# Kernel tuning notes

Hardware: AMD Instinct MI355X
Metric: run time of the kernel (lower is better)

## Reference

```python
import jax, jax.numpy as jnp
import numpy as np

N_NODES = 8192
N_EDGES = 32768
D = 768
H1 = 8
NEG_SLOPE = 0.2


def setup_inputs() -> dict:
    key = jax.random.key(0)
    ks = jax.random.split(key, 10)
    s = 0.02  # init scale keeps attention logits numerically tame
    x = jax.random.normal(ks[0], (N_NODES, D), dtype=jnp.float32)
    edge_index = jax.random.randint(ks[1], (2, N_EDGES), 0, N_NODES, dtype=jnp.int64)
    W1 = jax.random.normal(ks[2], (D, H1 * D), dtype=jnp.float32) * s
    a_src1 = jax.random.normal(ks[3], (H1, D), dtype=jnp.float32) * s
    a_dst1 = jax.random.normal(ks[4], (H1, D), dtype=jnp.float32) * s
    b1 = jnp.zeros((H1 * D,), dtype=jnp.float32)
    W2 = jax.random.normal(ks[5], (H1 * D, D), dtype=jnp.float32) * s
    a_src2 = jax.random.normal(ks[6], (1, D), dtype=jnp.float32) * s
    a_dst2 = jax.random.normal(ks[7], (1, D), dtype=jnp.float32) * s
    b2 = jnp.zeros((D,), dtype=jnp.float32)
    return {"x": x, "edge_index": edge_index, "W1": W1, "a_src1": a_src1,
            "a_dst1": a_dst1, "b1": b1, "W2": W2, "a_src2": a_src2,
            "a_dst2": a_dst2, "b2": b2}


def gat_conv(x, src, dst, W, a_src, a_dst, b, heads, out_ch):
    """PyG GATConv (concat=True, self-loops already appended to src/dst)."""
    n = x.shape[0]
    h = (x @ W).reshape(n, heads, out_ch)            # [N,H,C]
    alpha_src = jnp.einsum("nhc,hc->nh", h, a_src)  # [N,H]
    alpha_dst = jnp.einsum("nhc,hc->nh", h, a_dst)  # [N,H]
    # edge scores: leaky_relu(a_src.h_j + a_dst.h_i) for edge j->i
    e = jax.nn.leaky_relu(alpha_src[src] + alpha_dst[dst], NEG_SLOPE)  # [E,H]
    # segment softmax over incoming edges of each destination node
    m = jax.ops.segment_max(e, dst, num_segments=n)   # [N,H]
    m = jnp.where(jnp.isfinite(m), m, 0.0)
    p = jnp.exp(e - m[dst])                           # [E,H]
    denom = jax.ops.segment_sum(p, dst, num_segments=n)
    alpha = p / denom[dst]                            # [E,H]
    msg = h[src] * alpha[:, :, None]                  # [E,H,C] gather+weight
    out = jax.ops.segment_sum(msg, dst, num_segments=n)  # [N,H,C] scatter-add
    return out.reshape(n, heads * out_ch) + b


def reference(x, edge_index, W1, a_src1, a_dst1, b1, W2, a_src2, a_dst2, b2):
    n = x.shape[0]
    loops = jnp.arange(n, dtype=edge_index.dtype)
    src = jnp.concatenate([edge_index[0], loops])  # add_self_loops=True
    dst = jnp.concatenate([edge_index[1], loops])
    h = gat_conv(x, src, dst, W1, a_src1, a_dst1, b1, H1, D)
    h = jax.nn.elu(h)
    out = gat_conv(h, src, dst, W2, a_src2, a_dst2, b2, 1, D)
    return out
```

## Files before the change

### kernel.cpp

```cpp
#include <hip/hip_runtime.h>
#include <hip/hip_bf16.h>


#define N_NODES 8192
#define N_EDGES 32768
#define E_TOT   (N_EDGES + N_NODES)
#define D_IN    768
#define H1      8
#define HC1     (H1 * D_IN)
#define KSPLIT  4
#define KSLICE  (HC1 / KSPLIT)

typedef unsigned short ushort_t;
using short8  = __attribute__((ext_vector_type(8))) short;
using short4v = __attribute__((ext_vector_type(4))) short;
using floatx4 = __attribute__((ext_vector_type(4))) float;

__device__ __forceinline__ float bf2f(unsigned short u) {
  return __uint_as_float(((unsigned)u) << 16);
}
__device__ __forceinline__ unsigned short f2bf(float f) {
  unsigned u = __float_as_uint(f);
  unsigned r = (u + 0x7fffu + ((u >> 16) & 1u)) >> 16;
  return (unsigned short)r;
}

__device__ __forceinline__ void gll16(const ushort_t* g, ushort_t* l) {
  __builtin_amdgcn_global_load_lds(
      (const __attribute__((address_space(1))) void*)g,
      (__attribute__((address_space(3))) void*)l, 16, 0, 0);
}

__global__ __launch_bounds__(256) void frag_transpose_kernel(
    const float* __restrict__ W, ushort_t* __restrict__ out,
    int Kdim, int Ndim) {
  __shared__ float lds[64 * 65];
  const int bx = blockIdx.x;
  const int by = blockIdx.y;
  const int tid = threadIdx.x;
  const int n0 = bx * 64, k0 = by * 64;
  const int nn = tid & 63, kq = tid >> 6;
#pragma unroll
  for (int it = 0; it < 16; ++it) {
    int kk = it * 4 + kq;
    lds[kk * 65 + nn] = W[(size_t)(k0 + kk) * Ndim + n0 + nn];
  }
  __syncthreads();
  const int Ksub = Kdim >> 5;
#pragma unroll
  for (int it = 0; it < 2; ++it) {
    int idx = tid + 256 * it;
    int c = idx >> 6, l = idx & 63;
    int cn = c >> 1, ck = c & 1;
    int lrow = l & 15, lq = l >> 4;
    int n_loc = cn * 16 + lrow;
    int kb = ck * 32 + lq * 8;
    ushort_t v[8];
#pragma unroll
    for (int e = 0; e < 8; ++e) v[e] = f2bf(lds[(kb + e) * 65 + n_loc]);
    size_t chunk = (size_t)(bx * 4 + cn) * Ksub + (by * 2 + ck);
    *(short8*)(out + chunk * 512 + l * 8) = *(short8*)v;
  }
}

__global__ void prep_aw_kernel(const float* __restrict__ W1,
                               const float* __restrict__ aS,
                               const float* __restrict__ aD,
                               float* __restrict__ awS,
                               float* __restrict__ awD) {
  const int d = blockIdx.x;
  const int t = threadIdx.x;
  const float* row = W1 + (size_t)d * HC1;
  float ps[H1], pd[H1];
#pragma unroll
  for (int h = 0; h < H1; ++h) { ps[h] = 0.f; pd[h] = 0.f; }
#pragma unroll
  for (int h = 0; h < H1; ++h)
#pragma unroll
    for (int j = 0; j < 3; ++j) {
      int idx = h * 768 + j * 256 + t;
      float w = row[idx];
      ps[h] += w * aS[idx];
      pd[h] += w * aD[idx];
    }
#pragma unroll
  for (int h = 0; h < H1; ++h)
    for (int off = 32; off > 0; off >>= 1) {
      ps[h] += __shfl_down(ps[h], off, 64);
      pd[h] += __shfl_down(pd[h], off, 64);
    }
  __shared__ float red[2][4][H1];
  int w = t >> 6;
  if ((t & 63) == 0) {
#pragma unroll
    for (int h = 0; h < H1; ++h) { red[0][w][h] = ps[h]; red[1][w][h] = pd[h]; }
  }
  __syncthreads();
  if (t < H1)
    awS[d * H1 + t] = red[0][0][t] + red[0][1][t] + red[0][2][t] + red[0][3][t];
  else if (t >= 64 && t < 64 + H1) {
    int h = t - 64;
    awD[d * H1 + h] = red[1][0][h] + red[1][1][h] + red[1][2][h] + red[1][3][h];
  }
}

__global__ void node_prep_kernel(const float* __restrict__ x,
                                 const float* __restrict__ awS,
                                 const float* __restrict__ awD,
                                 ushort_t* __restrict__ xb,
                                 float* __restrict__ as1,
                                 float* __restrict__ ad1) {
  const int n = blockIdx.x;
  const int t = threadIdx.x;
  float ps[H1], pd[H1];
#pragma unroll
  for (int h = 0; h < H1; ++h) { ps[h] = 0.f; pd[h] = 0.f; }
#pragma unroll
  for (int j = 0; j < 3; ++j) {
    int d = j * 256 + t;
    float xv = x[(size_t)n * 768 + d];
    xb[(size_t)n * 768 + d] = f2bf(xv);
    const float4* s4 = (const float4*)(awS + d * 8);
    const float4* d4 = (const float4*)(awD + d * 8);
    float4 a0 = s4[0], a1 = s4[1];
    float4 c0 = d4[0], c1 = d4[1];
    ps[0] += xv * a0.x; ps[1] += xv * a0.y; ps[2] += xv * a0.z; ps[3] += xv * a0.w;
    ps[4] += xv * a1.x; ps[5] += xv * a1.y; ps[6] += xv * a1.z; ps[7] += xv * a1.w;
    pd[0] += xv * c0.x; pd[1] += xv * c0.y; pd[2] += xv * c0.z; pd[3] += xv * c0.w;
    pd[4] += xv * c1.x; pd[5] += xv * c1.y; pd[6] += xv * c1.z; pd[7] += xv * c1.w;
  }
#pragma unroll
  for (int h = 0; h < H1; ++h)
    for (int off = 32; off > 0; off >>= 1) {
      ps[h] += __shfl_down(ps[h], off, 64);
      pd[h] += __shfl_down(pd[h], off, 64);
    }
  __shared__ float red[2][4][H1];
  int w = t >> 6;
  if ((t & 63) == 0) {
#pragma unroll
    for (int h = 0; h < H1; ++h) { red[0][w][h] = ps[h]; red[1][w][h] = pd[h]; }
  }
  __syncthreads();
  if (t < H1)
    as1[n * H1 + t] = red[0][0][t] + red[0][1][t] + red[0][2][t] + red[0][3][t];
  else if (t >= 64 && t < 64 + H1) {
    int h = t - 64;
    ad1[n * H1 + h] = red[1][0][h] + red[1][1][h] + red[1][2][h] + red[1][3][h];
  }
}

__global__ void deg_kernel(const int* __restrict__ dst, int* __restrict__ deg) {
  int e = blockIdx.x * blockDim.x + threadIdx.x;
  if (e >= E_TOT) return;
  int d = (e < N_EDGES) ? dst[e] : (e - N_EDGES);
  atomicAdd(&deg[d], 1);
}

__global__ void scan_kernel(const int* __restrict__ deg, int* __restrict__ start,
                            int* __restrict__ cursor) {
  __shared__ int sums[1024];
  int t = threadIdx.x;
  int base = t * 8;
  int local[8];
  int s = 0;
#pragma unroll
  for (int i = 0; i < 8; ++i) { local[i] = s; s += deg[base + i]; }
  sums[t] = s;
  __syncthreads();
  for (int off = 1; off < 1024; off <<= 1) {
    int v = (t >= off) ? sums[t - off] : 0;
    __syncthreads();
    sums[t] += v;
    __syncthreads();
  }
  int excl = (t == 0) ? 0 : sums[t - 1];
#pragma unroll
  for (int i = 0; i < 8; ++i) {
    int st = excl + local[i];
    start[base + i] = st;
    cursor[base + i] = st;
  }
}

__global__ void fill_kernel(const int* __restrict__ dst, int* __restrict__ cursor,
                            int* __restrict__ csr) {
  int e = blockIdx.x * blockDim.x + threadIdx.x;
  if (e >= E_TOT) return;
  int d = (e < N_EDGES) ? dst[e] : (e - N_EDGES);
  int pos = atomicAdd(&cursor[d], 1);
  csr[pos] = e;
}

__global__ __launch_bounds__(256) void attn1_kernel(
    const ushort_t* __restrict__ xb, const float* __restrict__ as1,
    const float* __restrict__ ad1, const int* __restrict__ start,
    const int* __restrict__ deg, const int* __restrict__ csr,
    const int* __restrict__ src, ushort_t* __restrict__ z_sw) {
  const int n = blockIdx.x;
  const int t = threadIdx.x;
  const int st = start[n], dg = deg[n];
  const int h = t & 7, eloc = t >> 3;
  __shared__ float invd[H1];
  __shared__ float alphaS[16][H1];
  __shared__ int sidx[16];
  __shared__ float red[4][H1];
  __shared__ uint4 xs[16 * 96];

  const float adv = ad1[n * H1 + h];
  float pden = 0.f;
  for (int base = 0; base < dg; base += 32) {
    int ei = base + eloc;
    if (ei < dg) {
      int e = csr[st + ei];
      int s = (e < N_EDGES) ? src[e] : (e - N_EDGES);
      float l = as1[s * H1 + h] + adv;
      l = l > 0.f ? l : 0.2f * l;
      pden += __expf(l);
    }
  }
  pden += __shfl_down(pden, 8, 64);
  pden += __shfl_down(pden, 16, 64);
  pden += __shfl_down(pden, 32, 64);
  if ((t & 63) < 8) red[t >> 6][h] = pden;
  __syncthreads();
  if (t < 8) invd[t] = 1.0f / (red[0][t] + red[1][t] + red[2][t] + red[3][t]);
  __syncthreads();

  int hp[3], ip[3];
#pragma unroll
  for (int p = 0; p < 3; ++p) {
    int c8 = p * 256 + t;
    hp[p] = c8 / 96;
    ip[p] = c8 % 96;
  }
  float acc[3][8];
#pragma unroll
  for (int p = 0; p < 3; ++p)
#pragma unroll
    for (int e = 0; e < 8; ++e) acc[p][e] = 0.f;

  for (int base = 0; base < dg; base += 16) {
    int cnt = dg - base; if (cnt > 16) cnt = 16;
    if (t < 128 && eloc < cnt) {
      int e = csr[st + base + eloc];
      int s = (e < N_EDGES) ? src[e] : (e - N_EDGES);
      float l = as1[s * H1 + h] + adv;
      l = l > 0.f ? l : 0.2f * l;
      alphaS[eloc][h] = __expf(l) * invd[h];
      if (h == 0) sidx[eloc] = s;
    }
    __syncthreads();
#pragma unroll
    for (int j = 0; j < 6; ++j) {
      int idx = t + 256 * j;
      int row = idx / 96;
      if (row < cnt) {
        int col = idx - row * 96;
        xs[idx] = *(const uint4*)(xb + (size_t)sidx[row] * 768 + col * 8);
      }
    }
    __syncthreads();
    for (int ei = 0; ei < cnt; ++ei) {
      const uint4* xr = &xs[ei * 96];
#pragma unroll
      for (int p = 0; p < 3; ++p) {
        uint4 v = xr[ip[p]];
        float al = alphaS[ei][hp[p]];
        unsigned uu[4] = {v.x, v.y, v.z, v.w};
#pragma unroll
        for (int q = 0; q < 4; ++q) {
          acc[p][2 * q]     += al * __uint_as_float(uu[q] << 16);
          acc[p][2 * q + 1] += al * __uint_as_float(uu[q] & 0xffff0000u);
        }
      }
    }
    __syncthreads();
  }
#pragma unroll
  for (int p = 0; p < 3; ++p) {
    int c8 = p * 256 + t;
    int k = c8 * 8;
    size_t chunk = (size_t)(n >> 4) * 192 + (k >> 5);
    int word = ((k >> 3) & 3) * 16 + (n & 15);
    ushort_t v[8];
#pragma unroll
    for (int e = 0; e < 8; ++e) v[e] = f2bf(acc[p][e]);
    *(short8*)(z_sw + chunk * 512 + word * 8) = *(short8*)v;
  }
}

#define STAGE_RING(t)                                                          \
  {                                                                            \
    ushort_t* ld_ = smem + ((t) & 3) * 16384 + slot512;                        \
    _Pragma("unroll") for (int q_ = 0; q_ < 4; ++q_)                           \
        gll16(SRC + (((size_t)(cb[q_] + (t))) << 9) + lane8, ld_ + q_ * 512);  \
  }

#define GSTEP_BODY(s, VMSTR, NSV)                                             \
  {                                                                           \
    asm volatile("s_waitcnt vmcnt(" VMSTR ")" ::: "memory");                  \
    __builtin_amdgcn_s_barrier();                                             \
    const ushort_t* buf_ = smem + ((s) & 3) * 16384;                          \
    short8 af[8], bf[4];                                                      \
    _Pragma("unroll") for (int j_ = 0; j_ < 4; ++j_)                          \
        bf[j_] = *(const short8*)(buf_ + 8192 + (wn * 4 + j_) * 512 + lane8); \
    _Pragma("unroll") for (int i_ = 0; i_ < 4; ++i_)                          \
        af[i_] = *(const short8*)(buf_ + (wm * 8 + i_) * 512 + lane8);        \
    if ((s) + 3 < (NSV)) STAGE_RING((s) + 3)                                  \
    __builtin_amdgcn_s_setprio(1);                                            \
    _Pragma("unroll") for (int i_ = 0; i_ < 4; ++i_)                          \
        _Pragma("unroll") for (int j_ = 0; j_ < 4; ++j_)                      \
            acc[i_][j_] = __builtin_amdgcn_mfma_f32_16x16x32_bf16(            \
                af[i_], bf[j_], acc[i_][j_], 0, 0, 0);                        \
    __builtin_amdgcn_s_setprio(0);                                            \
    _Pragma("unroll") for (int i_ = 4; i_ < 8; ++i_)                          \
        af[i_] = *(const short8*)(buf_ + (wm * 8 + i_) * 512 + lane8);        \
    __builtin_amdgcn_s_barrier();                                             \
    __builtin_amdgcn_s_setprio(1);                                            \
    _Pragma("unroll") for (int i_ = 4; i_ < 8; ++i_)                          \
        _Pragma("unroll") for (int j_ = 0; j_ < 4; ++j_)                      \
            acc[i_][j_] = __builtin_amdgcn_mfma_f32_16x16x32_bf16(            \
                af[i_], bf[j_], acc[i_][j_], 0, 0, 0);                        \
    __builtin_amdgcn_s_setprio(0);                                            \
  }

#define GEMM_PIPE(NSV)                                                        \
  _Pragma("unroll") for (int p_ = 0; p_ < 3; ++p_) STAGE_RING(p_)             \
  _Pragma("unroll 2") for (int s_ = 0; s_ < (NSV)-2; ++s_) {                  \
    GSTEP_BODY(s_, "8", (NSV))                                                \
  }                                                                           \
  GSTEP_BODY((NSV)-2, "4", (NSV))                                             \
  GSTEP_BODY((NSV)-1, "0", (NSV))

__global__ __launch_bounds__(512, 2) void gemm_l1_kernel(
    const ushort_t* __restrict__ Asw, const ushort_t* __restrict__ Bsw,
    const float* __restrict__ biasb, ushort_t* __restrict__ Csw) {
  __shared__ ushort_t smem[4 * 16384];
  const int id = blockIdx.x;
  const int head = id & 7;
  const int j_id = id >> 3;
  const int n_t = j_id % 3;
  const int m_t = j_id / 3;
  const int tid = threadIdx.x;
  const int lane = tid & 63;
  const int w = tid >> 6;
  const int wm = w >> 2, wn = w & 3;
  const int lrow = lane & 15, lq = lane >> 4;
  const int lane8 = lane * 8;
  const int slot512 = w * 2048;
  const ushort_t* SRC = (w < 4) ? Asw : Bsw;

  int cb[4];
#pragma unroll
  for (int q = 0; q < 4; ++q) {
    int v;
    if (w < 4)
      v = (m_t * 16 + 4 * w + q) * 192 + head * 24;
    else
      v = (head * 48 + n_t * 16 + 4 * (w - 4) + q) * 24;
    cb[q] = __builtin_amdgcn_readfirstlane(v);
  }

  floatx4 acc[8][4];
#pragma unroll
  for (int i = 0; i < 8; ++i)
#pragma unroll
    for (int j = 0; j < 4; ++j) acc[i][j] = {0.f, 0.f, 0.f, 0.f};

  GEMM_PIPE(24)

  __syncthreads();
  ushort_t* tile = smem;
  const float* bias = biasb + head * 768 + n_t * 256;
#pragma unroll
  for (int p = 0; p < 2; ++p) {
    if (p) __syncthreads();
    if (wm == p) {
#pragma unroll
      for (int i = 0; i < 8; ++i)
#pragma unroll
        for (int j = 0; j < 4; ++j) {
          int col = wn * 64 + j * 16 + lrow;
          float bv = bias[col];
#pragma unroll
          for (int r = 0; r < 4; ++r) {
            float v = acc[i][j][r] + bv;
            v = v > 0.f ? v : __expf(v) - 1.0f;
            tile[(i * 16 + lq * 4 + r) * 280 + col] = f2bf(v);
          }
        }
    }
    __syncthreads();
#pragma unroll
    for (int cc = 0; cc < 8; ++cc) {
      int ch = w * 8 + cc;
      int RB = ch >> 3, kg = ch & 7;
      short8 vv =
          *(const short8*)&tile[(RB * 16 + lrow) * 280 + kg * 32 + lq * 8];
      size_t chunk_g = (size_t)(m_t * 16 + p * 8 + RB) * 192 + head * 24 +
                       n_t * 8 + kg;
      *((short8*)Csw + chunk_g * 64 + lane) = vv;
    }
  }
}

__global__ __launch_bounds__(512, 2) void gemm_l2_kernel(
    const ushort_t* __restrict__ Asw, const ushort_t* __restrict__ Bsw,
    float* __restrict__ Cp) {
  __shared__ ushort_t smem[4 * 16384];
  const int id = blockIdx.x;
  const int c = id & 7;
  const int sl = c >> 1;
  const int j_id = id >> 3;
  const int n_t = j_id % 3;
  const int m_t = (j_id / 3) * 2 + (c & 1);
  const int tid = threadIdx.x;
  const int lane = tid & 63;
  const int w = tid >> 6;
  const int wm = w >> 2, wn = w & 3;
  const int lrow = lane & 15, lq = lane >> 4;
  const int lane8 = lane * 8;
  const int slot512 = w * 2048;
  const ushort_t* SRC = (w < 4) ? Asw : Bsw;

  int cb[4];
#pragma unroll
  for (int q = 0; q < 4; ++q) {
    int v;
    if (w < 4)
      v = (m_t * 16 + 4 * w + q) * 192 + sl * 48;
    else
      v = (n_t * 16 + 4 * (w - 4) + q) * 192 + sl * 48;
    cb[q] = __builtin_amdgcn_readfirstlane(v);
  }

  floatx4 acc[8][4];
#pragma unroll
  for (int i = 0; i < 8; ++i)
#pragma unroll
    for (int j = 0; j < 4; ++j) acc[i][j] = {0.f, 0.f, 0.f, 0.f};

  GEMM_PIPE(48)

  float* C = Cp + (size_t)sl * N_NODES * 768;
  const int m0 = m_t * 256, n0 = n_t * 256;
#pragma unroll
  for (int i = 0; i < 8; ++i) {
    int row_b = m0 + wm * 128 + i * 16 + lq * 4;
#pragma unroll
    for (int j = 0; j < 4; ++j) {
      int col = n0 + wn * 64 + j * 16 + lrow;
#pragma unroll
      for (int r = 0; r < 4; ++r)
        C[(size_t)(row_b + r) * 768 + col] = acc[i][j][r];
    }
  }
}

__global__ __launch_bounds__(192) void reduce_alpha2_kernel(
    const float* __restrict__ parts, const float* __restrict__ aS,
    const float* __restrict__ aD, ushort_t* __restrict__ yb,
    float* __restrict__ as2, float* __restrict__ ad2) {
  const int n = blockIdx.x;
  const int t = threadIdx.x;
  const size_t S = (size_t)N_NODES * 768;
  const size_t base = (size_t)n * 768 + t * 4;
  float4 v0 = *(const float4*)(parts + base);
  float4 v1 = *(const float4*)(parts + base + S);
  float4 v2 = *(const float4*)(parts + base + 2 * S);
  float4 v3 = *(const float4*)(parts + base + 3 * S);
  float vx = v0.x + v1.x + v2.x + v3.x;
  float vy = v0.y + v1.y + v2.y + v3.y;
  float vz = v0.z + v1.z + v2.z + v3.z;
  float vw = v0.w + v1.w + v2.w + v3.w;
  short4v pb = {(short)f2bf(vx), (short)f2bf(vy), (short)f2bf(vz),
                (short)f2bf(vw)};
  *(short4v*)(yb + base) = pb;
  const float4 a4 = *(const float4*)(aS + t * 4);
  const float4 d4 = *(const float4*)(aD + t * 4);
  float ps = vx * a4.x + vy * a4.y + vz * a4.z + vw * a4.w;
  float pd = vx * d4.x + vy * d4.y + vz * d4.z + vw * d4.w;
  for (int off = 32; off > 0; off >>= 1) {
    ps += __shfl_down(ps, off, 64);
    pd += __shfl_down(pd, off, 64);
  }
  __shared__ float red[2][3];
  int w = t >> 6;
  if ((t & 63) == 0) { red[0][w] = ps; red[1][w] = pd; }
  __syncthreads();
  if (t == 0) as2[n] = red[0][0] + red[0][1] + red[0][2];
  if (t == 64) ad2[n] = red[1][0] + red[1][1] + red[1][2];
}

__global__ __launch_bounds__(384) void attn2_kernel(
    const ushort_t* __restrict__ yb, const float* __restrict__ as2,
    const float* __restrict__ ad2, const int* __restrict__ start,
    const int* __restrict__ deg, const int* __restrict__ csr,
    const int* __restrict__ src, const float* __restrict__ b2,
    float* __restrict__ out) {
  const int n = blockIdx.x;
  const int t = threadIdx.x;
  const int st = start[n], dg = deg[n];
  __shared__ float alphaS[64];
  __shared__ int sidx[64];
  __shared__ float red[6];
  __shared__ float invd_sh;

  const float adv = ad2[n];
  float pden = 0.f;
  for (int ei = t; ei < dg; ei += 384) {
    int e = csr[st + ei];
    int s = (e < N_EDGES) ? src[e] : (e - N_EDGES);
    float l = as2[s] + adv;
    l = l > 0.f ? l : 0.2f * l;
    pden += __expf(l);
  }
  for (int off = 32; off > 0; off >>= 1) pden += __shfl_down(pden, off, 64);
  if ((t & 63) == 0) red[t >> 6] = pden;
  __syncthreads();
  if (t == 0)
    invd_sh = 1.0f /
              (red[0] + red[1] + red[2] + red[3] + red[4] + red[5]);
  __syncthreads();
  const float invd = invd_sh;

  float a0 = 0.f, a1 = 0.f;
  for (int base = 0; base < dg; base += 64) {
    int cnt = dg - base; if (cnt > 64) cnt = 64;
    if (t < cnt) {
      int e = csr[st + base + t];
      int s = (e < N_EDGES) ? src[e] : (e - N_EDGES);
      float l = as2[s] + adv;
      l = l > 0.f ? l : 0.2f * l;
      alphaS[t] = __expf(l) * invd;
      sidx[t] = s;
    }
    __syncthreads();
    for (int ei = 0; ei < cnt; ++ei) {
      float al = alphaS[ei];
      unsigned u = *(const unsigned*)(yb + (size_t)sidx[ei] * 768 + 2 * t);
      a0 += al * __uint_as_float(u << 16);
      a1 += al * __uint_as_float(u & 0xffff0000u);
    }
    __syncthreads();
  }
  const float2 b = *(const float2*)(b2 + 2 * t);
  float2 o;
  o.x = a0 + b.x;
  o.y = a1 + b.y;
  *(float2*)(out + (size_t)n * 768 + 2 * t) = o;
}

extern "C" void kernel_launch(void* const* d_in, const int* in_sizes, int n_in,
                              void* d_out, int out_size, void* d_ws, size_t ws_size,
                              hipStream_t stream) {
  const float* x      = (const float*)d_in[0];
  const int*   ei     = (const int*)d_in[1];
  const float* W1     = (const float*)d_in[2];
  const float* a_src1 = (const float*)d_in[3];
  const float* a_dst1 = (const float*)d_in[4];
  const float* b1     = (const float*)d_in[5];
  const float* W2     = (const float*)d_in[6];
  const float* a_src2 = (const float*)d_in[7];
  const float* a_dst2 = (const float*)d_in[8];
  const float* b2     = (const float*)d_in[9];
  float* out = (float*)d_out;
  const int* src = ei;
  const int* dst = ei + N_EDGES;

  char* ws = (char*)d_ws;
  size_t off = 0;
  auto alloc = [&](size_t bytes) -> void* {
    void* p = ws + off;
    off = (off + bytes + 255) & ~(size_t)255;
    return p;
  };

  int* deg = (int*)alloc(N_NODES * 4);
  float* awS = (float*)alloc(768 * H1 * 4);
  float* awD = (float*)alloc(768 * H1 * 4);
  float* as1 = (float*)alloc(N_NODES * H1 * 4);
  float* ad1 = (float*)alloc(N_NODES * H1 * 4);
  float* as2 = (float*)alloc(N_NODES * 4);
  float* ad2 = (float*)alloc(N_NODES * 4);
  int* start  = (int*)alloc(N_NODES * 4);
  int* cursor = (int*)alloc(N_NODES * 4);
  int* csr    = (int*)alloc(E_TOT * 4);
  ushort_t* xb     = (ushort_t*)alloc((size_t)N_NODES * D_IN * 2);
  ushort_t* w1t_sw = (ushort_t*)alloc((size_t)HC1 * D_IN * 2 + 8192);
  ushort_t* w2t_sw = (ushort_t*)alloc((size_t)HC1 * D_IN * 2 + 8192);
  ushort_t* z_sw   = (ushort_t*)alloc((size_t)N_NODES * HC1 * 2 + 8192);
  ushort_t* h2b_sw = (ushort_t*)alloc((size_t)N_NODES * HC1 * 2 + 8192);
  ushort_t* yb  = xb;
  float* parts  = (float*)z_sw;
  (void)ws_size; (void)n_in; (void)in_sizes; (void)out_size;

  hipMemsetAsync(deg, 0, N_NODES * 4, stream);

  prep_aw_kernel<<<768, 256, 0, stream>>>(W1, a_src1, a_dst1, awS, awD);
  node_prep_kernel<<<N_NODES, 256, 0, stream>>>(x, awS, awD, xb, as1, ad1);
  frag_transpose_kernel<<<dim3(HC1 / 64, D_IN / 64), 256, 0, stream>>>(
      W1, w1t_sw, D_IN, HC1);
  frag_transpose_kernel<<<dim3(D_IN / 64, HC1 / 64), 256, 0, stream>>>(
      W2, w2t_sw, HC1, D_IN);

  deg_kernel<<<(E_TOT + 255) / 256, 256, 0, stream>>>(dst, deg);
  scan_kernel<<<1, 1024, 0, stream>>>(deg, start, cursor);
  fill_kernel<<<(E_TOT + 255) / 256, 256, 0, stream>>>(dst, cursor, csr);

  attn1_kernel<<<N_NODES, 256, 0, stream>>>(xb, as1, ad1, start, deg, csr,
                                            src, z_sw);
  gemm_l1_kernel<<<8 * 32 * 3, 512, 0, stream>>>(z_sw, w1t_sw, b1, h2b_sw);

  gemm_l2_kernel<<<KSPLIT * 2 * 16 * 3, 512, 0, stream>>>(h2b_sw, w2t_sw,
                                                          parts);
  reduce_alpha2_kernel<<<N_NODES, 192, 0, stream>>>(parts, a_src2, a_dst2, yb,
                                                    as2, ad2);
  attn2_kernel<<<N_NODES, 384, 0, stream>>>(yb, as2, ad2, start, deg, csr,
                                            src, b2, out);
}
```

Measured before the change: 477.1 us.

## Halve GEMM N-tile to 256x128, double-buffer LDS, fuse aw prep into W1 transpose

Both bf16 MFMA GEMMs move from a 256x256 tile with a 4-stage LDS ring to a 256x128 tile with a 2-stage double buffer. This cuts LDS use and accumulator registers so launch bounds can ask for 4 blocks per CU instead of 2, and it doubles the grid. The cost is more redundant A-tile loads and a shallower prefetch, since each step waits on vmcnt(0). Separately, the W1·a_src/a_dst projection is folded into the W1 fragment-transpose kernel, reusing the tile already staged in LDS and accumulating per-head sums with atomics after memsets, which removes a separate pass over W1.

```diff
diff --git a/kernel.cpp b/kernel.cpp
--- a/kernel.cpp
+++ b/kernel.cpp
@@ -63,44 +63,52 @@
   }
 }
 
-__global__ void prep_aw_kernel(const float* __restrict__ W1,
-                               const float* __restrict__ aS,
-                               const float* __restrict__ aD,
-                               float* __restrict__ awS,
-                               float* __restrict__ awD) {
-  const int d = blockIdx.x;
-  const int t = threadIdx.x;
-  const float* row = W1 + (size_t)d * HC1;
-  float ps[H1], pd[H1];
-#pragma unroll
-  for (int h = 0; h < H1; ++h) { ps[h] = 0.f; pd[h] = 0.f; }
-#pragma unroll
-  for (int h = 0; h < H1; ++h)
-#pragma unroll
-    for (int j = 0; j < 3; ++j) {
-      int idx = h * 768 + j * 256 + t;
-      float w = row[idx];
-      ps[h] += w * aS[idx];
-      pd[h] += w * aD[idx];
-    }
-#pragma unroll
-  for (int h = 0; h < H1; ++h)
-    for (int off = 32; off > 0; off >>= 1) {
-      ps[h] += __shfl_down(ps[h], off, 64);
-      pd[h] += __shfl_down(pd[h], off, 64);
-    }
-  __shared__ float red[2][4][H1];
-  int w = t >> 6;
-  if ((t & 63) == 0) {
-#pragma unroll
-    for (int h = 0; h < H1; ++h) { red[0][w][h] = ps[h]; red[1][w][h] = pd[h]; }
-  }
-  __syncthreads();
-  if (t < H1)
-    awS[d * H1 + t] = red[0][0][t] + red[0][1][t] + red[0][2][t] + red[0][3][t];
-  else if (t >= 64 && t < 64 + H1) {
-    int h = t - 64;
-    awD[d * H1 + h] = red[1][0][h] + red[1][1][h] + red[1][2][h] + red[1][3][h];
+__global__ __launch_bounds__(256) void frag_transpose_aw_kernel(
+    const float* __restrict__ W, ushort_t* __restrict__ out,
+    const float* __restrict__ aS, const float* __restrict__ aD,
+    float* __restrict__ awS, float* __restrict__ awD) {
+  __shared__ float lds[64 * 65];
+  const int bx = blockIdx.x;
+  const int by = blockIdx.y;
+  const int tid = threadIdx.x;
+  const int n0 = bx * 64, k0 = by * 64;
+  const int nn = tid & 63, kq = tid >> 6;
+#pragma unroll
+  for (int it = 0; it < 16; ++it) {
+    int kk = it * 4 + kq;
+    lds[kk * 65 + nn] = W[(size_t)(k0 + kk) * 6144 + n0 + nn];
+  }
+  __syncthreads();
+#pragma unroll
+  for (int it = 0; it < 2; ++it) {
+    int idx = tid + 256 * it;
+    int c = idx >> 6, l = idx & 63;
+    int cn = c >> 1, ck = c & 1;
+    int lrow = l & 15, lq = l >> 4;
+    int n_loc = cn * 16 + lrow;
+    int kb = ck * 32 + lq * 8;
+    ushort_t v[8];
+#pragma unroll
+    for (int e = 0; e < 8; ++e) v[e] = f2bf(lds[(kb + e) * 65 + n_loc]);
+    size_t chunk = (size_t)(bx * 4 + cn) * 24 + (by * 2 + ck);
+    *(short8*)(out + chunk * 512 + l * 8) = *(short8*)v;
+  }
+  const int r = tid >> 2, nq = tid & 3;
+  float s_ = 0.f, d_ = 0.f;
+  const float* aSp = aS + n0 + nq * 16;
+  const float* aDp = aD + n0 + nq * 16;
+#pragma unroll
+  for (int c = 0; c < 16; ++c) {
+    float v = lds[r * 65 + nq * 16 + c];
+    s_ += v * aSp[c];
+    d_ += v * aDp[c];
+  }
+  s_ += __shfl_down(s_, 2, 4); s_ += __shfl_down(s_, 1, 4);
+  d_ += __shfl_down(d_, 2, 4); d_ += __shfl_down(d_, 1, 4);
+  if (nq == 0) {
+    int h = n0 / 768;
+    atomicAdd(&awS[(k0 + r) * H1 + h], s_);
+    atomicAdd(&awD[(k0 + r) * H1 + h], d_);
   }
 }
 
@@ -290,65 +298,53 @@
   }
 }
 
-#define STAGE_RING(t)                                                          \
-  {                                                                            \
-    ushort_t* ld_ = smem + ((t) & 3) * 16384 + slot512;                        \
-    _Pragma("unroll") for (int q_ = 0; q_ < 4; ++q_)                           \
-        gll16(SRC + (((size_t)(cb[q_] + (t))) << 9) + lane8, ld_ + q_ * 512);  \
-  }
-
-#define GSTEP_BODY(s, VMSTR, NSV)                                             \
+#define STAGE2(t)                                                             \
   {                                                                           \
-    asm volatile("s_waitcnt vmcnt(" VMSTR ")" ::: "memory");                  \
+    ushort_t* ld_ = smem + ((t) & 1) * 12288 + slotu;                         \
+    for (int q_ = 0; q_ < nst; ++q_)                                          \
+      gll16(SRC + (((size_t)(cb[q_] + (t))) << 9) + lane8, ld_ + q_ * 512);   \
+  }
+
+#define GSTEPX(s, NSV)                                                        \
+  {                                                                           \
+    asm volatile("s_waitcnt vmcnt(0)" ::: "memory");                          \
     __builtin_amdgcn_s_barrier();                                             \
-    const ushort_t* buf_ = smem + ((s) & 3) * 16384;                          \
-    short8 af[8], bf[4];                                                      \
+    if ((s) + 1 < (NSV)) STAGE2((s) + 1)                                      \
+    const ushort_t* buf_ = smem + ((s) & 1) * 12288;                          \
+    short8 af[4], bf[4];                                                      \
+    _Pragma("unroll") for (int i_ = 0; i_ < 4; ++i_)                          \
+        af[i_] = *(const short8*)(buf_ + (wm * 4 + i_) * 512 + lane8);        \
     _Pragma("unroll") for (int j_ = 0; j_ < 4; ++j_)                          \
         bf[j_] = *(const short8*)(buf_ + 8192 + (wn * 4 + j_) * 512 + lane8); \
-    _Pragma("unroll") for (int i_ = 0; i_ < 4; ++i_)                          \
-        af[i_] = *(const short8*)(buf_ + (wm * 8 + i_) * 512 + lane8);        \
-    if ((s) + 3 < (NSV)) STAGE_RING((s) + 3)                                  \
     __builtin_amdgcn_s_setprio(1);                                            \
     _Pragma("unroll") for (int i_ = 0; i_ < 4; ++i_)                          \
-        _Pragma("unroll") for (int j_ = 0; j_ < 4; ++j_)                      \
-            acc[i_][j_] = __builtin_amdgcn_mfma_f32_16x16x32_bf16(            \
-                af[i_], bf[j_], acc[i_][j_], 0, 0, 0);                        \
+      _Pragma("unroll") for (int j_ = 0; j_ < 4; ++j_)                        \
+        acc[i_][j_] = __builtin_amdgcn_mfma_f32_16x16x32_bf16(                \
+            af[i_], bf[j_], acc[i_][j_], 0, 0, 0);                            \
     __builtin_amdgcn_s_setprio(0);                                            \
-    _Pragma("unroll") for (int i_ = 4; i_ < 8; ++i_)                          \
-        af[i_] = *(const short8*)(buf_ + (wm * 8 + i_) * 512 + lane8);        \
-    __builtin_amdgcn_s_barrier();                                             \
-    __builtin_amdgcn_s_setprio(1);                                            \
-    _Pragma("unroll") for (int i_ = 4; i_ < 8; ++i_)                          \
-        _Pragma("unroll") for (int j_ = 0; j_ < 4; ++j_)                      \
-            acc[i_][j_] = __builtin_amdgcn_mfma_f32_16x16x32_bf16(            \
-                af[i_], bf[j_], acc[i_][j_], 0, 0, 0);                        \
-    __builtin_amdgcn_s_setprio(0);                                            \
-  }
-
-#define GEMM_PIPE(NSV)                                                        \
-  _Pragma("unroll") for (int p_ = 0; p_ < 3; ++p_) STAGE_RING(p_)             \
-  _Pragma("unroll 2") for (int s_ = 0; s_ < (NSV)-2; ++s_) {                  \
-    GSTEP_BODY(s_, "8", (NSV))                                                \
-  }                                                                           \
-  GSTEP_BODY((NSV)-2, "4", (NSV))                                             \
-  GSTEP_BODY((NSV)-1, "0", (NSV))
-
-__global__ __launch_bounds__(512, 2) void gemm_l1_kernel(
+  }
+
+#define GEMM_PIPEX(NSV)                                                       \
+  STAGE2(0)                                                                   \
+  _Pragma("unroll 2") for (int s_ = 0; s_ < (NSV); ++s_) { GSTEPX(s_, (NSV)) }
+
+__global__ __launch_bounds__(512, 4) void gemm_l1_kernel(
     const ushort_t* __restrict__ Asw, const ushort_t* __restrict__ Bsw,
     const float* __restrict__ biasb, ushort_t* __restrict__ Csw) {
-  __shared__ ushort_t smem[4 * 16384];
+  __shared__ ushort_t smem[24576];
   const int id = blockIdx.x;
   const int head = id & 7;
   const int j_id = id >> 3;
-  const int n_t = j_id % 3;
-  const int m_t = j_id / 3;
+  const int n_t = j_id % 6;
+  const int m_t = j_id / 6;
   const int tid = threadIdx.x;
   const int lane = tid & 63;
   const int w = tid >> 6;
-  const int wm = w >> 2, wn = w & 3;
+  const int wm = w >> 1, wn = w & 1;
   const int lrow = lane & 15, lq = lane >> 4;
   const int lane8 = lane * 8;
-  const int slot512 = w * 2048;
+  const int nst = (w < 4) ? 4 : 2;
+  const int slotu = (w < 4) ? w * 2048 : 8192 + (w - 4) * 1024;
   const ushort_t* SRC = (w < 4) ? Asw : Bsw;
 
   int cb[4];
@@ -358,27 +354,27 @@
     if (w < 4)
       v = (m_t * 16 + 4 * w + q) * 192 + head * 24;
     else
-      v = (head * 48 + n_t * 16 + 4 * (w - 4) + q) * 24;
+      v = (head * 48 + n_t * 8 + 2 * (w - 4) + (q & 1)) * 24;
     cb[q] = __builtin_amdgcn_readfirstlane(v);
   }
 
-  floatx4 acc[8][4];
-#pragma unroll
-  for (int i = 0; i < 8; ++i)
+  floatx4 acc[4][4];
+#pragma unroll
+  for (int i = 0; i < 4; ++i)
 #pragma unroll
     for (int j = 0; j < 4; ++j) acc[i][j] = {0.f, 0.f, 0.f, 0.f};
 
-  GEMM_PIPE(24)
+  GEMM_PIPEX(24)
 
   __syncthreads();
   ushort_t* tile = smem;
-  const float* bias = biasb + head * 768 + n_t * 256;
-#pragma unroll
-  for (int p = 0; p < 2; ++p) {
-    if (p) __syncthreads();
-    if (wm == p) {
-#pragma unroll
-      for (int i = 0; i < 8; ++i)
+  const float* bias = biasb + head * 768 + n_t * 128;
+#pragma unroll
+  for (int q4 = 0; q4 < 4; ++q4) {
+    if (q4) __syncthreads();
+    if (wm == q4) {
+#pragma unroll
+      for (int i = 0; i < 4; ++i)
 #pragma unroll
         for (int j = 0; j < 4; ++j) {
           int col = wn * 64 + j * 16 + lrow;
@@ -387,41 +383,42 @@
           for (int r = 0; r < 4; ++r) {
             float v = acc[i][j][r] + bv;
             v = v > 0.f ? v : __expf(v) - 1.0f;
-            tile[(i * 16 + lq * 4 + r) * 280 + col] = f2bf(v);
+            tile[(i * 16 + lq * 4 + r) * 136 + col] = f2bf(v);
           }
         }
     }
     __syncthreads();
 #pragma unroll
-    for (int cc = 0; cc < 8; ++cc) {
-      int ch = w * 8 + cc;
-      int RB = ch >> 3, kg = ch & 7;
+    for (int cc = 0; cc < 2; ++cc) {
+      int ch = w * 2 + cc;
+      int RB = ch >> 2, kg = ch & 3;
       short8 vv =
-          *(const short8*)&tile[(RB * 16 + lrow) * 280 + kg * 32 + lq * 8];
-      size_t chunk_g = (size_t)(m_t * 16 + p * 8 + RB) * 192 + head * 24 +
-                       n_t * 8 + kg;
+          *(const short8*)&tile[(RB * 16 + lrow) * 136 + kg * 32 + lq * 8];
+      size_t chunk_g = (size_t)(m_t * 16 + q4 * 4 + RB) * 192 + head * 24 +
+                       n_t * 4 + kg;
       *((short8*)Csw + chunk_g * 64 + lane) = vv;
     }
   }
 }
 
-__global__ __launch_bounds__(512, 2) void gemm_l2_kernel(
+__global__ __launch_bounds__(512, 4) void gemm_l2_kernel(
     const ushort_t* __restrict__ Asw, const ushort_t* __restrict__ Bsw,
     float* __restrict__ Cp) {
-  __shared__ ushort_t smem[4 * 16384];
+  __shared__ ushort_t smem[24576];
   const int id = blockIdx.x;
   const int c = id & 7;
   const int sl = c >> 1;
   const int j_id = id >> 3;
-  const int n_t = j_id % 3;
-  const int m_t = (j_id / 3) * 2 + (c & 1);
+  const int n_t = j_id % 6;
+  const int m_t = (j_id / 6) * 2 + (c & 1);
   const int tid = threadIdx.x;
   const int lane = tid & 63;
   const int w = tid >> 6;
-  const int wm = w >> 2, wn = w & 3;
+  const int wm = w >> 1, wn = w & 1;
   const int lrow = lane & 15, lq = lane >> 4;
   const int lane8 = lane * 8;
-  const int slot512 = w * 2048;
+  const int nst = (w < 4) ? 4 : 2;
+  const int slotu = (w < 4) ? w * 2048 : 8192 + (w - 4) * 1024;
   const ushort_t* SRC = (w < 4) ? Asw : Bsw;
 
   int cb[4];
@@ -431,23 +428,23 @@
     if (w < 4)
       v = (m_t * 16 + 4 * w + q) * 192 + sl * 48;
     else
-      v = (n_t * 16 + 4 * (w - 4) + q) * 192 + sl * 48;
+      v = (n_t * 8 + 2 * (w - 4) + (q & 1)) * 192 + sl * 48;
     cb[q] = __builtin_amdgcn_readfirstlane(v);
   }
 
-  floatx4 acc[8][4];
-#pragma unroll
-  for (int i = 0; i < 8; ++i)
+  floatx4 acc[4][4];
+#pragma unroll
+  for (int i = 0; i < 4; ++i)
 #pragma unroll
     for (int j = 0; j < 4; ++j) acc[i][j] = {0.f, 0.f, 0.f, 0.f};
 
-  GEMM_PIPE(48)
+  GEMM_PIPEX(48)
 
   float* C = Cp + (size_t)sl * N_NODES * 768;
-  const int m0 = m_t * 256, n0 = n_t * 256;
-#pragma unroll
-  for (int i = 0; i < 8; ++i) {
-    int row_b = m0 + wm * 128 + i * 16 + lq * 4;
+  const int m0 = m_t * 256, n0 = n_t * 128;
+#pragma unroll
+  for (int i = 0; i < 4; ++i) {
+    int row_b = m0 + wm * 64 + i * 16 + lq * 4;
 #pragma unroll
     for (int j = 0; j < 4; ++j) {
       int col = n0 + wn * 64 + j * 16 + lrow;
@@ -597,13 +594,14 @@
   (void)ws_size; (void)n_in; (void)in_sizes; (void)out_size;
 
   hipMemsetAsync(deg, 0, N_NODES * 4, stream);
-
-  prep_aw_kernel<<<768, 256, 0, stream>>>(W1, a_src1, a_dst1, awS, awD);
-  node_prep_kernel<<<N_NODES, 256, 0, stream>>>(x, awS, awD, xb, as1, ad1);
-  frag_transpose_kernel<<<dim3(HC1 / 64, D_IN / 64), 256, 0, stream>>>(
-      W1, w1t_sw, D_IN, HC1);
+  hipMemsetAsync(awS, 0, 768 * H1 * 4, stream);
+  hipMemsetAsync(awD, 0, 768 * H1 * 4, stream);
+
+  frag_transpose_aw_kernel<<<dim3(HC1 / 64, D_IN / 64), 256, 0, stream>>>(
+      W1, w1t_sw, a_src1, a_dst1, awS, awD);
   frag_transpose_kernel<<<dim3(D_IN / 64, HC1 / 64), 256, 0, stream>>>(
       W2, w2t_sw, HC1, D_IN);
+  node_prep_kernel<<<N_NODES, 256, 0, stream>>>(x, awS, awD, xb, as1, ad1);
 
   deg_kernel<<<(E_TOT + 255) / 256, 256, 0, stream>>>(dst, deg);
   scan_kernel<<<1, 1024, 0, stream>>>(deg, start, cursor);
@@ -611,9 +609,9 @@
 
   attn1_kernel<<<N_NODES, 256, 0, stream>>>(xb, as1, ad1, start, deg, csr,
                                             src, z_sw);
-  gemm_l1_kernel<<<8 * 32 * 3, 512, 0, stream>>>(z_sw, w1t_sw, b1, h2b_sw);
-
-  gemm_l2_kernel<<<KSPLIT * 2 * 16 * 3, 512, 0, stream>>>(h2b_sw, w2t_sw,
+  gemm_l1_kernel<<<8 * 32 * 6, 512, 0, stream>>>(z_sw, w1t_sw, b1, h2b_sw);
+
+  gemm_l2_kernel<<<KSPLIT * 2 * 16 * 6, 512, 0, stream>>>(h2b_sw, w2t_sw,
                                                           parts);
   reduce_alpha2_kernel<<<N_NODES, 192, 0, stream>>>(parts, a_src2, a_dst2, yb,
                                                     as2, ad2);
```

Result: slower. 487.7 us (+2.2%).
